# Kernel tuning notes

Hardware: AMD Instinct MI355X
Metric: run time of the kernel (lower is better)

## Reference

```python
import jax, jax.numpy as jnp
import numpy as np

B, S, D, A = 32, 2048, 512, 256


def setup_inputs() -> dict:
    key = jax.random.key(0)
    ks = jax.random.split(key, 9)
    enc = jax.random.normal(ks[0], (B, S, D), dtype=jnp.float32)
    dec = jax.random.normal(ks[1], (B, 1, D), dtype=jnp.float32)
    prev = jax.random.uniform(ks[2], (B, S), dtype=jnp.float32)
    prev = prev / jnp.sum(prev, axis=1, keepdims=True)  # normalized prev attention
    noise = jax.random.normal(ks[3], (B, S), dtype=jnp.float32)
    W = jax.random.normal(ks[4], (A, D), dtype=jnp.float32) / np.sqrt(D)
    V = jax.random.normal(ks[5], (A, D), dtype=jnp.float32) / np.sqrt(D)
    b = jax.random.normal(ks[6], (A,), dtype=jnp.float32)
    v_w = jax.random.normal(ks[7], (1, A), dtype=jnp.float32)
    v_g = jnp.full((1,), np.sqrt(1.0 / A), dtype=jnp.float32)  # weight_norm g init
    v_bias = jax.random.normal(ks[8], (1,), dtype=jnp.float32)
    r = jnp.full((1,), -4.0, dtype=jnp.float32)
    return {"encoder_outputs": enc, "decoder_h": dec, "prev_alpha": prev,
            "noise": noise, "W": W, "V": V, "b": b, "v_w": v_w,
            "v_g": v_g, "v_bias": v_bias, "r": r}


def reference(encoder_outputs, decoder_h, prev_alpha, noise, W, V, b, v_w, v_g, v_bias, r):
    # Energy: tanh-MLP Bahdanau score with weight-normed output projection
    h = jnp.tanh(jnp.einsum('bsd,ad->bsa', encoder_outputs, W)
                 + jnp.einsum('bod,ad->boa', decoder_h, V)  # [B,1,A] broadcasts over S
                 + b)
    w_eff = v_g * v_w / jnp.linalg.norm(v_w)       # weight_norm: g * v / ||v||
    energy = jnp.einsum('bsa,oa->bso', h, w_eff)[..., 0] + v_bias[0] + r[0]  # [B,S]
    # Soft monotonic attention recurrence
    p_select = jax.nn.sigmoid(energy + noise)
    log1mp = jnp.log(jnp.clip(1.0 - p_select, 1e-10, 1.0))
    cumprod_1mp = jnp.exp(jnp.cumsum(log1mp, axis=1))  # safe_cumprod
    alpha = p_select * cumprod_1mp * jnp.cumsum(prev_alpha / cumprod_1mp, axis=1)
    # Context: enc^T @ alpha
    context = jnp.einsum('bsd,bs->bd', encoder_outputs, alpha)
    return context, alpha
```

## Files before the change

kernel.cpp:

```cpp
#include <hip/hip_runtime.h>
#include <math.h>

#define B_  32
#define S_  2048
#define D_  512
#define A_  256
#define BS_ (B_ * S_)

#define WEFF_OFF  0
#define DEC_OFF   256
#define EPART_OFF 8448
#define CTX_OFF   (8448 + BS_)

typedef _Float16 f16x8 __attribute__((ext_vector_type(8)));
typedef __fp16   fp16x2 __attribute__((ext_vector_type(2)));
typedef _Float16 half4 __attribute__((ext_vector_type(4)));
typedef float floatx4 __attribute__((ext_vector_type(4)));

__device__ __forceinline__ void glds16(const void* g, void* l) {
    __builtin_amdgcn_global_load_lds(
        (const __attribute__((address_space(1))) void*)g,
        (__attribute__((address_space(3))) void*)l, 16, 0, 0);
}

__global__ void ma_prep_kernel(const float* __restrict__ v_w,
                               const float* __restrict__ v_g,
                               const float* __restrict__ dec,
                               const float* __restrict__ V,
                               const float* __restrict__ bvec,
                               const float* __restrict__ W,
                               _Float16* __restrict__ W16,
                               float* __restrict__ ws) {
    __shared__ float sh[D_];
    const int bid = blockIdx.x, t = threadIdx.x;
    if (bid == 0) {
        float v = v_w[t];
        float sq = v * v;
        #pragma unroll
        for (int off = 32; off > 0; off >>= 1) sq += __shfl_down(sq, off, 64);
        if ((t & 63) == 0) sh[t >> 6] = sq;
        __syncthreads();
        float n2 = sh[0] + sh[1] + sh[2] + sh[3];
        ws[WEFF_OFF + t] = v_g[0] * v / sqrtf(n2);
    } else if (bid <= B_) {
        const int b = bid - 1;
        sh[t]       = dec[b * D_ + t];
        sh[t + 256] = dec[b * D_ + 256 + t];
        __syncthreads();
        const float4* Vr = (const float4*)(V + (size_t)t * D_);
        float acc = 0.f;
        #pragma unroll 4
        for (int k = 0; k < D_ / 4; ++k) {
            float4 v4 = Vr[k];
            acc = fmaf(v4.x, sh[4*k+0], acc);
            acc = fmaf(v4.y, sh[4*k+1], acc);
            acc = fmaf(v4.z, sh[4*k+2], acc);
            acc = fmaf(v4.w, sh[4*k+3], acc);
        }
        ws[DEC_OFF + b * A_ + t] = acc + bvec[t];
    } else {
        int i = (bid - (B_ + 1)) * 256 + t;
        float4 v = ((const float4*)W)[i];
        half4 h;
        h[0] = (_Float16)v.x; h[1] = (_Float16)v.y;
        h[2] = (_Float16)v.z; h[3] = (_Float16)v.w;
        ((half4*)W16)[i] = h;
    }
}

__global__ __launch_bounds__(256) void ma_energy_mfma(
        const float* __restrict__ enc,
        const _Float16* __restrict__ W16,
        const float* __restrict__ ws_in,
        float* __restrict__ energy) {
    __shared__ __align__(16) float    As[2][64 * 32];
    __shared__ __align__(16) _Float16 Bs[2][256 * 32];
    __shared__ float red[4][64];

    const int t  = threadIdx.x;
    const int bx = blockIdx.x;
    const size_t R0 = (size_t)bx * 64;
    const int batch = bx >> 5;

    const int lane = t & 63, wn = t >> 6;
    const int fr = lane & 15, kq = lane >> 4;

    const int ar = t >> 3, ac = t & 7;
    const float* AgS0 = enc + (R0 + (size_t)ar) * D_ + (ac ^ (ar & 7)) * 4;
    const float* AgS1 = AgS0 + (size_t)32 * D_;
    const int br = t >> 2, bc = t & 3;
    const _Float16* BgS = W16 + (size_t)br * D_ + (bc ^ ((br >> 1) & 3)) * 8;

    const int axc0 = ((2 * kq)     ^ (fr & 7)) * 4;
    const int axc1 = ((2 * kq + 1) ^ (fr & 7)) * 4;
    const int bxo  = (kq ^ ((fr >> 1) & 3)) * 8;

    floatx4 acc[4][4];
    #pragma unroll
    for (int m = 0; m < 4; ++m)
        #pragma unroll
        for (int n = 0; n < 4; ++n) acc[m][n] = (floatx4)0.f;

    glds16(AgS0, &As[0][t * 4]);
    glds16(AgS1, &As[0][(t + 256) * 4]);
    #pragma unroll
    for (int j = 0; j < 4; ++j)
        glds16(BgS + (size_t)j * 64 * D_, &Bs[0][(j * 256 + t) * 8]);
    __syncthreads();

    #pragma unroll 1
    for (int kt = 0; kt < 16; ++kt) {
        const int cur = kt & 1;
        if (kt < 15) {
            const int nxt = cur ^ 1;
            const int ko = (kt + 1) * 32;
            glds16(AgS0 + ko, &As[nxt][t * 4]);
            glds16(AgS1 + ko, &As[nxt][(t + 256) * 4]);
            #pragma unroll
            for (int j = 0; j < 4; ++j)
                glds16(BgS + (size_t)j * 64 * D_ + ko, &Bs[nxt][(j * 256 + t) * 8]);
        }
        f16x8 af[4];
        #pragma unroll
        for (int m = 0; m < 4; ++m) {
            const int rbase = (m * 16 + fr) * 32;
            float4 lo = *(const float4*)&As[cur][rbase + axc0];
            float4 hi = *(const float4*)&As[cur][rbase + axc1];
            union { fp16x2 h2[4]; f16x8 v; } u;
            u.h2[0] = __builtin_amdgcn_cvt_pkrtz(lo.x, lo.y);
            u.h2[1] = __builtin_amdgcn_cvt_pkrtz(lo.z, lo.w);
            u.h2[2] = __builtin_amdgcn_cvt_pkrtz(hi.x, hi.y);
            u.h2[3] = __builtin_amdgcn_cvt_pkrtz(hi.z, hi.w);
            af[m] = u.v;
        }
        f16x8 bf[4];
        #pragma unroll
        for (int n = 0; n < 4; ++n)
            bf[n] = *(const f16x8*)&Bs[cur][(wn * 64 + n * 16 + fr) * 32 + bxo];
        #pragma unroll
        for (int m = 0; m < 4; ++m)
            #pragma unroll
            for (int n = 0; n < 4; ++n)
                acc[m][n] = __builtin_amdgcn_mfma_f32_16x16x32_f16(af[m], bf[n], acc[m][n], 0, 0, 0);
        __syncthreads();
    }

    const float* weff  = ws_in + WEFF_OFF;
    const float* dterm = ws_in + DEC_OFF + batch * A_;
    float wj[4], dj[4];
    #pragma unroll
    for (int n = 0; n < 4; ++n) {
        int a = wn * 64 + n * 16 + fr;
        wj[n] = weff[a];
        dj[n] = dterm[a];
    }
    #pragma unroll
    for (int m = 0; m < 4; ++m) {
        #pragma unroll
        for (int r = 0; r < 4; ++r) {
            float v = 0.f;
            #pragma unroll
            for (int n = 0; n < 4; ++n) {
                float x = acc[m][n][r] + dj[n];
                float e = __expf(2.f * x);
                v += (1.f - 2.f / (e + 1.f)) * wj[n];
            }
            #pragma unroll
            for (int mask = 1; mask < 16; mask <<= 1)
                v += __shfl_xor(v, mask, 64);
            if (fr == 0)
                red[wn][m * 16 + (kq << 2) + r] = v;
        }
    }
    __syncthreads();
    if (t < 64)
        energy[R0 + t] = red[0][t] + red[1][t] + red[2][t] + red[3][t];
}

__global__ void ma_scan_kernel(const float* __restrict__ energy,
                               const float* __restrict__ noise,
                               const float* __restrict__ prev,
                               const float* __restrict__ v_bias,
                               const float* __restrict__ r,
                               float* __restrict__ alpha_out) {
    int b = blockIdx.x, t = threadIdx.x;
    const float bias = v_bias[0] + r[0];
    int base = b * S_ + t * 8;
    float p[8], av[8], bv[8];
    #pragma unroll
    for (int i = 0; i < 8; ++i) {
        float e = energy[base + i] + bias + noise[base + i];
        float pi = 1.f / (1.f + expf(-e));
        p[i]  = pi;
        av[i] = fmaxf(1.f - pi, 1e-10f);
        bv[i] = prev[base + i];
    }
    float Ai = 1.f, Bi = 0.f;
    #pragma unroll
    for (int i = 0; i < 8; ++i) { Bi = av[i] * Bi + bv[i]; Ai *= av[i]; }
    int lane = t & 63;
    #pragma unroll
    for (int off = 1; off < 64; off <<= 1) {
        float Ap = __shfl_up(Ai, off, 64);
        float Bp = __shfl_up(Bi, off, 64);
        if (lane >= off) { Bi = Ai * Bp + Bi; Ai = Ai * Ap; }
    }
    __shared__ float wA[4], wB[4];
    int w = t >> 6;
    if (lane == 63) { wA[w] = Ai; wB[w] = Bi; }
    __syncthreads();
    float Ax = __shfl_up(Ai, 1, 64);
    float Bx = __shfl_up(Bi, 1, 64);
    if (lane == 0) { Ax = 1.f; Bx = 0.f; }
    float PwA = 1.f, PwB = 0.f;
    for (int q = 0; q < w; ++q) { PwB = wA[q] * PwB + wB[q]; PwA *= wA[q]; }
    float T = Ax * PwB + Bx;
    #pragma unroll
    for (int i = 0; i < 8; ++i) {
        T = av[i] * T + bv[i];
        alpha_out[base + i] = p[i] * T;
    }
}

__global__ void ma_ctxpart_kernel(const float* __restrict__ enc,
                                  const float* __restrict__ alpha,
                                  float* __restrict__ cpart) {
    int b = blockIdx.x, sc = blockIdx.y, t = threadIdx.x;
    const int sp = t >> 7;
    const int d4 = t & 127;
    const float4* e = (const float4*)(enc + ((size_t)b * S_ + sc * 128) * D_);
    const float* al = alpha + b * S_ + sc * 128;
    float4 acc = {0.f, 0.f, 0.f, 0.f};
    #pragma unroll 4
    for (int s = sp; s < 128; s += 2) {
        float a = al[s];
        float4 v = e[(size_t)s * 128 + d4];
        acc.x = fmaf(v.x, a, acc.x);
        acc.y = fmaf(v.y, a, acc.y);
        acc.z = fmaf(v.z, a, acc.z);
        acc.w = fmaf(v.w, a, acc.w);
    }
    __shared__ float4 sh[128];
    if (sp == 1) sh[d4] = acc;
    __syncthreads();
    if (sp == 0) {
        float4 o = sh[d4];
        acc.x += o.x; acc.y += o.y; acc.z += o.z; acc.w += o.w;
        ((float4*)(cpart + ((size_t)(sc * B_ + b)) * D_))[d4] = acc;
    }
}

__global__ void ma_ctxreduce_kernel(const float* __restrict__ cpart,
                                    float* __restrict__ ctx) {
    int b = blockIdx.x, d = threadIdx.x;
    float s = 0.f;
    #pragma unroll
    for (int q = 0; q < 16; ++q) s += cpart[((size_t)(q * B_ + b)) * D_ + d];
    ctx[b * D_ + d] = s;
}

extern "C" void kernel_launch(void* const* d_in, const int* in_sizes, int n_in,
                              void* d_out, int out_size, void* d_ws, size_t ws_size,
                              hipStream_t stream) {
    const float* enc    = (const float*)d_in[0];
    const float* dec    = (const float*)d_in[1];
    const float* prev   = (const float*)d_in[2];
    const float* noise  = (const float*)d_in[3];
    const float* W      = (const float*)d_in[4];
    const float* V      = (const float*)d_in[5];
    const float* bvec   = (const float*)d_in[6];
    const float* v_w    = (const float*)d_in[7];
    const float* v_g    = (const float*)d_in[8];
    const float* v_bias = (const float*)d_in[9];
    const float* r      = (const float*)d_in[10];

    float* out = (float*)d_out;
    float* ws  = (float*)d_ws;
    float* alpha = out + B_ * D_;
    _Float16* W16 = (_Float16*)(ws + CTX_OFF);

    ma_prep_kernel<<<1 + B_ + 128, 256, 0, stream>>>(v_w, v_g, dec, V, bvec, W, W16, ws);
    ma_energy_mfma<<<1024, 256, 0, stream>>>(enc, W16, ws, ws + EPART_OFF);
    ma_scan_kernel<<<B_, 256, 0, stream>>>(ws + EPART_OFF, noise, prev, v_bias, r, alpha);
    dim3 gc(B_, 16);
    ma_ctxpart_kernel<<<gc, 256, 0, stream>>>(enc, alpha, ws + CTX_OFF);
    ma_ctxreduce_kernel<<<B_, 512, 0, stream>>>(ws + CTX_OFF, out);
}
```

Baseline: 89.07 us.

## Retile energy GEMM to 128x128 tiles split over A panels with fp16 LDS staging

The energy GEMM block tile changes from 64 rows x 256 A-columns to 128 rows x 128 A-columns. Each block handles one of two A panels and writes partial energies to a doubled workspace, and the scan kernel sums the two partials. The A operand is now loaded through registers, converted to fp16 once and stored to LDS as fp16, rather than copied as fp32 and converted on every fragment read. This halves LDS use and adds a launch bound asking for 3 blocks per CU, aiming at better occupancy and less redundant conversion. The cost is that each encoder row is read from global memory twice (once per panel), plus an extra partial-energy buffer.

```diff
diff --git a/kernel.cpp b/kernel.cpp
--- a/kernel.cpp
+++ b/kernel.cpp
@@ -10,7 +10,7 @@
 #define WEFF_OFF  0
 #define DEC_OFF   256
 #define EPART_OFF 8448
-#define CTX_OFF   (8448 + BS_)
+#define CTX_OFF   (8448 + 2 * BS_)
 
 typedef _Float16 f16x8 __attribute__((ext_vector_type(8)));
 typedef __fp16   fp16x2 __attribute__((ext_vector_type(2)));
@@ -68,32 +68,35 @@
     }
 }
 
-__global__ __launch_bounds__(256) void ma_energy_mfma(
+__global__ __launch_bounds__(256, 3) void ma_energy_mfma(
         const float* __restrict__ enc,
         const _Float16* __restrict__ W16,
         const float* __restrict__ ws_in,
-        float* __restrict__ energy) {
-    __shared__ __align__(16) float    As[2][64 * 32];
-    __shared__ __align__(16) _Float16 Bs[2][256 * 32];
-    __shared__ float red[4][64];
+        float* __restrict__ epart) {
+    __shared__ __align__(16) _Float16 As[2][128 * 32];
+    __shared__ __align__(16) _Float16 Bs[2][128 * 32];
 
     const int t  = threadIdx.x;
     const int bx = blockIdx.x;
-    const size_t R0 = (size_t)bx * 64;
-    const int batch = bx >> 5;
-
-    const int lane = t & 63, wn = t >> 6;
+    const int rt = bx >> 1, panel = bx & 1;
+    const size_t R0 = (size_t)rt * 128;
+    const int batch = rt >> 4;
+
+    const int lane = t & 63, wid = t >> 6;
+    const int wm = wid >> 1, wn = wid & 1;
     const int fr = lane & 15, kq = lane >> 4;
 
-    const int ar = t >> 3, ac = t & 7;
-    const float* AgS0 = enc + (R0 + (size_t)ar) * D_ + (ac ^ (ar & 7)) * 4;
-    const float* AgS1 = AgS0 + (size_t)32 * D_;
+    const int ar = t >> 1, ah = t & 1;
+    const float* Ag = enc + (R0 + (size_t)ar) * D_ + ah * 16;
+    const int asw  = (ar >> 1) & 3;
+    const int awc0 = ((2 * ah)     ^ asw) * 8;
+    const int awc1 = ((2 * ah + 1) ^ asw) * 8;
+
     const int br = t >> 2, bc = t & 3;
-    const _Float16* BgS = W16 + (size_t)br * D_ + (bc ^ ((br >> 1) & 3)) * 8;
-
-    const int axc0 = ((2 * kq)     ^ (fr & 7)) * 4;
-    const int axc1 = ((2 * kq + 1) ^ (fr & 7)) * 4;
-    const int bxo  = (kq ^ ((fr >> 1) & 3)) * 8;
+    const _Float16* BgS = W16 + (size_t)(panel * 128 + br) * D_
+                              + ((bc ^ ((br >> 1) & 3)) * 8);
+
+    const int fxo = (kq ^ ((fr >> 1) & 3)) * 8;
 
     floatx4 acc[4][4];
     #pragma unroll
@@ -101,56 +104,71 @@
         #pragma unroll
         for (int n = 0; n < 4; ++n) acc[m][n] = (floatx4)0.f;
 
-    glds16(AgS0, &As[0][t * 4]);
-    glds16(AgS1, &As[0][(t + 256) * 4]);
-    #pragma unroll
-    for (int j = 0; j < 4; ++j)
-        glds16(BgS + (size_t)j * 64 * D_, &Bs[0][(j * 256 + t) * 8]);
+    float4 pa[4];
+
+#define LOADA(kt) do { \
+        _Pragma("unroll") \
+        for (int j = 0; j < 4; ++j) \
+            pa[j] = *(const float4*)(Ag + (kt) * 32 + j * 4); \
+    } while (0)
+
+#define STOREA(buf) do { \
+        union { fp16x2 h2[4]; f16x8 v; } u0, u1; \
+        u0.h2[0] = __builtin_amdgcn_cvt_pkrtz(pa[0].x, pa[0].y); \
+        u0.h2[1] = __builtin_amdgcn_cvt_pkrtz(pa[0].z, pa[0].w); \
+        u0.h2[2] = __builtin_amdgcn_cvt_pkrtz(pa[1].x, pa[1].y); \
+        u0.h2[3] = __builtin_amdgcn_cvt_pkrtz(pa[1].z, pa[1].w); \
+        u1.h2[0] = __builtin_amdgcn_cvt_pkrtz(pa[2].x, pa[2].y); \
+        u1.h2[1] = __builtin_amdgcn_cvt_pkrtz(pa[2].z, pa[2].w); \
+        u1.h2[2] = __builtin_amdgcn_cvt_pkrtz(pa[3].x, pa[3].y); \
+        u1.h2[3] = __builtin_amdgcn_cvt_pkrtz(pa[3].z, pa[3].w); \
+        *(f16x8*)&As[buf][ar * 32 + awc0] = u0.v; \
+        *(f16x8*)&As[buf][ar * 32 + awc1] = u1.v; \
+    } while (0)
+
+#define STAGEB(kt, buf) do { \
+        glds16(BgS + (kt) * 32,                 &Bs[buf][t * 8]); \
+        glds16(BgS + (size_t)64 * D_ + (kt) * 32, &Bs[buf][(256 + t) * 8]); \
+    } while (0)
+
+    STAGEB(0, 0);
+    LOADA(0);
+    STOREA(0);
     __syncthreads();
 
     #pragma unroll 1
     for (int kt = 0; kt < 16; ++kt) {
         const int cur = kt & 1;
         if (kt < 15) {
-            const int nxt = cur ^ 1;
-            const int ko = (kt + 1) * 32;
-            glds16(AgS0 + ko, &As[nxt][t * 4]);
-            glds16(AgS1 + ko, &As[nxt][(t + 256) * 4]);
-            #pragma unroll
-            for (int j = 0; j < 4; ++j)
-                glds16(BgS + (size_t)j * 64 * D_ + ko, &Bs[nxt][(j * 256 + t) * 8]);
+            STAGEB(kt + 1, cur ^ 1);
+            LOADA(kt + 1);
         }
-        f16x8 af[4];
-        #pragma unroll
-        for (int m = 0; m < 4; ++m) {
-            const int rbase = (m * 16 + fr) * 32;
-            float4 lo = *(const float4*)&As[cur][rbase + axc0];
-            float4 hi = *(const float4*)&As[cur][rbase + axc1];
-            union { fp16x2 h2[4]; f16x8 v; } u;
-            u.h2[0] = __builtin_amdgcn_cvt_pkrtz(lo.x, lo.y);
-            u.h2[1] = __builtin_amdgcn_cvt_pkrtz(lo.z, lo.w);
-            u.h2[2] = __builtin_amdgcn_cvt_pkrtz(hi.x, hi.y);
-            u.h2[3] = __builtin_amdgcn_cvt_pkrtz(hi.z, hi.w);
-            af[m] = u.v;
-        }
-        f16x8 bf[4];
+        f16x8 af[4], bf[4];
+        #pragma unroll
+        for (int m = 0; m < 4; ++m)
+            af[m] = *(const f16x8*)&As[cur][(wm * 64 + m * 16 + fr) * 32 + fxo];
         #pragma unroll
         for (int n = 0; n < 4; ++n)
-            bf[n] = *(const f16x8*)&Bs[cur][(wn * 64 + n * 16 + fr) * 32 + bxo];
+            bf[n] = *(const f16x8*)&Bs[cur][(wn * 64 + n * 16 + fr) * 32 + fxo];
         #pragma unroll
         for (int m = 0; m < 4; ++m)
             #pragma unroll
             for (int n = 0; n < 4; ++n)
                 acc[m][n] = __builtin_amdgcn_mfma_f32_16x16x32_f16(af[m], bf[n], acc[m][n], 0, 0, 0);
+        if (kt < 15) STOREA(cur ^ 1);
         __syncthreads();
     }
-
+#undef LOADA
+#undef STOREA
+#undef STAGEB
+
+    float* const red = (float*)As;
     const float* weff  = ws_in + WEFF_OFF;
     const float* dterm = ws_in + DEC_OFF + batch * A_;
     float wj[4], dj[4];
     #pragma unroll
     for (int n = 0; n < 4; ++n) {
-        int a = wn * 64 + n * 16 + fr;
+        int a = panel * 128 + wn * 64 + n * 16 + fr;
         wj[n] = weff[a];
         dj[n] = dterm[a];
     }
@@ -169,15 +187,15 @@
             for (int mask = 1; mask < 16; mask <<= 1)
                 v += __shfl_xor(v, mask, 64);
             if (fr == 0)
-                red[wn][m * 16 + (kq << 2) + r] = v;
+                red[wn * 128 + wm * 64 + m * 16 + (kq << 2) + r] = v;
         }
     }
     __syncthreads();
-    if (t < 64)
-        energy[R0 + t] = red[0][t] + red[1][t] + red[2][t] + red[3][t];
-}
-
-__global__ void ma_scan_kernel(const float* __restrict__ energy,
+    if (t < 128)
+        epart[(size_t)panel * BS_ + R0 + t] = red[t] + red[128 + t];
+}
+
+__global__ void ma_scan_kernel(const float* __restrict__ epart,
                                const float* __restrict__ noise,
                                const float* __restrict__ prev,
                                const float* __restrict__ v_bias,
@@ -189,7 +207,7 @@
     float p[8], av[8], bv[8];
     #pragma unroll
     for (int i = 0; i < 8; ++i) {
-        float e = energy[base + i] + bias + noise[base + i];
+        float e = epart[base + i] + epart[BS_ + base + i] + bias + noise[base + i];
         float pi = 1.f / (1.f + expf(-e));
         p[i]  = pi;
         av[i] = fmaxf(1.f - pi, 1e-10f);
```

After: 92.51 us. +3.9%, slower.
